# Kernel optimization log

Measured on AMD Instinct MI355X. Metric: run time of the kernel, lower is better.

Reference implementation:

```python
import jax, jax.numpy as jnp
import numpy as np

B, T, C = 2, 2048, 1024
NH = 16
DFF = 4096
EPS = 1e-5


def setup_inputs() -> dict:
    key = jax.random.key(0)
    ks = jax.random.split(key, 12)
    s = 0.02
    return {
        "x": jax.random.normal(ks[0], (B, T, C), dtype=jnp.float32),
        "Wq": jax.random.normal(ks[1], (C, C), dtype=jnp.float32) * s,
        "bq": jax.random.normal(ks[2], (C,), dtype=jnp.float32) * s,
        "Wk": jax.random.normal(ks[3], (C, C), dtype=jnp.float32) * s,
        "bk": jax.random.normal(ks[4], (C,), dtype=jnp.float32) * s,
        "Wv": jax.random.normal(ks[5], (C, C), dtype=jnp.float32) * s,
        "bv": jax.random.normal(ks[6], (C,), dtype=jnp.float32) * s,
        "W1": jax.random.normal(ks[7], (C, DFF), dtype=jnp.float32) * s,
        "b1": jax.random.normal(ks[8], (DFF,), dtype=jnp.float32) * s,
        "W2": jax.random.normal(ks[9], (DFF, C), dtype=jnp.float32) * s,
        "b2": jax.random.normal(ks[10], (C,), dtype=jnp.float32) * s,
        "ln_w": jnp.ones((C,), dtype=jnp.float32),
    }


def _layernorm(x, w):
    # LayerNorm over last dim, weight only (bias=False), eps=1e-5
    mu = jnp.mean(x, axis=-1, keepdims=True)
    var = jnp.mean(jnp.square(x - mu), axis=-1, keepdims=True)
    return (x - mu) / jnp.sqrt(var + EPS) * w


def reference(x, Wq, bq, Wk, bk, Wv, bv, W1, b1, W2, b2, ln_w):
    Bx, Tx, Cx = x.shape
    hd = Cx // NH
    q = (x @ Wq + bq).reshape(Bx, Tx, NH, hd).transpose(0, 2, 1, 3)  # [B,H,T,hd]
    k = (x @ Wk + bk).reshape(Bx, Tx, NH, hd).transpose(0, 2, 1, 3)
    v = (x @ Wv + bv).reshape(Bx, Tx, NH, hd).transpose(0, 2, 1, 3)
    # NOTE: original scales by sqrt(d_k) = sqrt(FULL model dim C), not head dim
    scores = jnp.einsum("bhqd,bhkd->bhqk", q, k) / jnp.sqrt(jnp.float32(Cx))
    causal = jnp.tril(jnp.ones((Tx, Tx), dtype=bool))
    scores = jnp.where(causal[None, None, :, :], scores, -jnp.inf)
    attn = jax.nn.softmax(scores, axis=-1)
    head_out = jnp.einsum("bhqk,bhkd->bhqd", attn, v)
    a = head_out.transpose(0, 2, 1, 3).reshape(Bx, Tx, Cx)
    # residuals: out = x + ln(x) with SHARED ln weight
    h = a + _layernorm(a, ln_w)
    f = jax.nn.relu(h @ W1 + b1) @ W2 + b2
    out = f + _layernorm(f, ln_w)
    return out
```

## Files before the change

kernel.cpp:

```cpp
#include <hip/hip_runtime.h>
#include <math.h>


typedef __attribute__((ext_vector_type(8))) short short8;
typedef __attribute__((ext_vector_type(4))) float f32x4;

__device__ __forceinline__ unsigned short f2bf(float f) {
    unsigned u = __builtin_bit_cast(unsigned, f);
    unsigned r = u + 0x7fffu + ((u >> 16) & 1u);
    return (unsigned short)(r >> 16);
}

__global__ __launch_bounds__(256) void convert_bf16_kernel(
    const float* __restrict__ in, unsigned short* __restrict__ out)
{
    const int i = (blockIdx.x * 256 + threadIdx.x) * 4;
    float4 v = *(const float4*)(in + i);
    ushort4 o;
    o.x = f2bf(v.x); o.y = f2bf(v.y); o.z = f2bf(v.z); o.w = f2bf(v.w);
    *(ushort4*)(out + i) = o;
}

__global__ __launch_bounds__(256) void transpose_convert_kernel(
    const float* __restrict__ in, unsigned short* __restrict__ out, int K, int N)
{
    __shared__ float tile[32][33];
    const int tx = threadIdx.x & 31;
    const int ty = threadIdx.x >> 5;
    const int n0 = blockIdx.x * 32;
    const int k0 = blockIdx.y * 32;
#pragma unroll
    for (int i = 0; i < 4; ++i)
        tile[ty + i * 8][tx] = in[(size_t)(k0 + ty + i * 8) * N + n0 + tx];
    __syncthreads();
#pragma unroll
    for (int i = 0; i < 4; ++i)
        out[(size_t)(n0 + ty + i * 8) * K + k0 + tx] = f2bf(tile[tx][ty + i * 8]);
}

__global__ __launch_bounds__(256) void concat2_kernel(
    const float* __restrict__ a, const float* __restrict__ b, float* __restrict__ o)
{
    const int i = blockIdx.x * 256 + threadIdx.x;
    o[i] = i < 1024 ? a[i] : b[i - 1024];
}

template <int TM, int TN>
__global__ __launch_bounds__(256) void gemm_bf16_mfma(
    const unsigned short* __restrict__ A, const unsigned short* __restrict__ Bt,
    const float* __restrict__ bias, float* __restrict__ Cf,
    unsigned short* __restrict__ Cb, int M, int N, int K, int mode)
{
    constexpr int NI = TM / 32;
    constexpr int NJ = TN / 32;
    constexpr int NA = TM / 64;
    constexpr int NB = TN / 64;

    __shared__ unsigned short As[TM * 32];
    __shared__ unsigned short Bs[TN * 32];

    const int tid  = threadIdx.x;
    const int lane = tid & 63;
    const int w    = tid >> 6;
    const int wm   = (w & 1) * (TM / 2);
    const int wn   = (w >> 1) * (TN / 2);
    const int fm   = lane & 15;
    const int quad = lane >> 4;

    const int row0 = blockIdx.y * TM;
    const int col0 = blockIdx.x * TN;

    const int srow = lane >> 2;
    const int scol = (lane & 3) * 8;

    const unsigned short* aptr[NA];
    unsigned short* alds[NA];
#pragma unroll
    for (int i = 0; i < NA; ++i) {
        const int r = (w * NA + i) * 16;
        aptr[i] = A + (size_t)(row0 + r + srow) * K + scol;
        alds[i] = &As[r * 32];
    }
    const unsigned short* bptr[NB];
    unsigned short* blds[NB];
#pragma unroll
    for (int i = 0; i < NB; ++i) {
        const int r = (w * NB + i) * 16;
        bptr[i] = Bt + (size_t)(col0 + r + srow) * K + scol;
        blds[i] = &Bs[r * 32];
    }

    f32x4 acc[NI][NJ] = {};

    for (int k0 = 0; k0 < K; k0 += 32) {
        __syncthreads();
#pragma unroll
        for (int i = 0; i < NA; ++i)
            __builtin_amdgcn_global_load_lds(
                (const __attribute__((address_space(1))) void*)(aptr[i] + k0),
                (__attribute__((address_space(3))) void*)alds[i], 16, 0, 0);
#pragma unroll
        for (int i = 0; i < NB; ++i)
            __builtin_amdgcn_global_load_lds(
                (const __attribute__((address_space(1))) void*)(bptr[i] + k0),
                (__attribute__((address_space(3))) void*)blds[i], 16, 0, 0);
        __syncthreads();

        short8 af[NI], bf[NJ];
#pragma unroll
        for (int i = 0; i < NI; ++i)
            af[i] = *(const short8*)&As[(wm + i * 16 + fm) * 32 + quad * 8];
#pragma unroll
        for (int j = 0; j < NJ; ++j)
            bf[j] = *(const short8*)&Bs[(wn + j * 16 + fm) * 32 + quad * 8];
#pragma unroll
        for (int i = 0; i < NI; ++i)
#pragma unroll
            for (int j = 0; j < NJ; ++j)
                acc[i][j] = __builtin_amdgcn_mfma_f32_16x16x32_bf16(
                    af[i], bf[j], acc[i][j], 0, 0, 0);
    }

#pragma unroll
    for (int j = 0; j < NJ; ++j) {
        const int col = col0 + wn + j * 16 + fm;
        const float bcol = (mode == 3) ? 0.f : bias[col];
#pragma unroll
        for (int i = 0; i < NI; ++i) {
            const int rbase = row0 + wm + i * 16 + quad * 4;
#pragma unroll
            for (int r = 0; r < 4; ++r) {
                const int row = rbase + r;
                float val = acc[i][j][r] + ((mode == 3) ? bias[row] : bcol);
                if (mode == 1) val = fmaxf(val, 0.f);
                if (mode == 0) Cf[(size_t)row * N + col] = val;
                else           Cb[(size_t)row * N + col] = f2bf(val);
            }
        }
    }
}

__global__ __launch_bounds__(256) void fattn_mfma(
    const unsigned short* __restrict__ qk,
    const unsigned short* __restrict__ vt,
    float* __restrict__ a)
{
    const int T = 2048, LDQK = 2048, LDVT = 4096, OUTC = 1024;
    const float cs = 0.04508422f;

    __shared__ unsigned short Qs[2][64][32];
    __shared__ unsigned short Ks[2][64][32];
    __shared__ unsigned short Vs[2][64][32];
    __shared__ unsigned short Ps[4][16][72];

    const int tid  = threadIdx.x;
    const int lane = tid & 63;
    const int w    = tid >> 6;
    const int fm   = lane & 15;
    const int quad = lane >> 4;
    const int srow = lane >> 2;
    const int scol = (lane & 3) * 8;

    const int n  = blockIdx.x;
    const int lo = n & 255, hi = n >> 8;
    const int h  = ((lo >> 5) & 7) | ((hi & 1) << 3);
    const int b  = hi >> 1;
    const int qv = lo & 31;
    const int u  = ((qv & 1) << 4) | ((qv & 2) << 2) | (qv & 4) |
                   ((qv & 8) >> 2) | ((qv & 16) >> 4);
    const int qb = (hi & 1) ? (31 - u) : u;
    const int q0 = qb * 64;

    const size_t rowbase = (size_t)b * T;

#pragma unroll
    for (int i = 0; i < 2; ++i) {
        const int c  = w * 2 + i;
        const int kh = c & 1, rg = c >> 1;
        const unsigned short* src = qk + (rowbase + q0 + rg * 16 + srow) * LDQK
                                       + h * 64 + kh * 32 + scol;
        __builtin_amdgcn_global_load_lds(
            (const __attribute__((address_space(1))) void*)src,
            (__attribute__((address_space(3))) void*)&Qs[kh][rg * 16][0], 16, 0, 0);
    }
    __syncthreads();
    short8 qf0 = *(const short8*)&Qs[0][w * 16 + fm][quad * 8];
    short8 qf1 = *(const short8*)&Qs[1][w * 16 + fm][quad * 8];

    short8 ones;
#pragma unroll
    for (int i = 0; i < 8; ++i) ones[i] = (short)0x3F80;

    f32x4 o[4] = {};
    f32x4 lacc = {};

    const int qglob = q0 + w * 16 + fm;

    for (int jt = 0; jt <= qb; ++jt) {
        const int j0 = jt * 64;
        __syncthreads();
#pragma unroll
        for (int i = 0; i < 2; ++i) {
            const int c  = w * 2 + i;
            const int kh = c & 1, rg = c >> 1;
            const unsigned short* ksrc = qk + (rowbase + j0 + rg * 16 + srow) * LDQK
                                            + 1024 + h * 64 + kh * 32 + scol;
            __builtin_amdgcn_global_load_lds(
                (const __attribute__((address_space(1))) void*)ksrc,
                (__attribute__((address_space(3))) void*)&Ks[kh][rg * 16][0], 16, 0, 0);
            const unsigned short* vsrc = vt + (size_t)(h * 64 + rg * 16 + srow) * LDVT
                                            + rowbase + j0 + kh * 32 + scol;
            __builtin_amdgcn_global_load_lds(
                (const __attribute__((address_space(1))) void*)vsrc,
                (__attribute__((address_space(3))) void*)&Vs[kh][rg * 16][0], 16, 0, 0);
        }
        __syncthreads();

        f32x4 s[4];
#pragma unroll
        for (int j = 0; j < 4; ++j) {
            short8 k0 = *(const short8*)&Ks[0][j * 16 + fm][quad * 8];
            short8 k1 = *(const short8*)&Ks[1][j * 16 + fm][quad * 8];
            f32x4 acc = {};
            acc = __builtin_amdgcn_mfma_f32_16x16x32_bf16(k0, qf0, acc, 0, 0, 0);
            acc = __builtin_amdgcn_mfma_f32_16x16x32_bf16(k1, qf1, acc, 0, 0, 0);
            s[j] = acc;
        }

        if (jt == qb) {
#pragma unroll
            for (int j = 0; j < 4; ++j) {
                const int kbase = j0 + j * 16 + quad * 4;
#pragma unroll
                for (int r = 0; r < 4; ++r) {
                    const float e = exp2f(s[j][r] * cs);
                    s[j][r] = (kbase + r > qglob) ? 0.f : e;
                }
            }
        } else {
#pragma unroll
            for (int j = 0; j < 4; ++j)
#pragma unroll
                for (int r = 0; r < 4; ++r)
                    s[j][r] = exp2f(s[j][r] * cs);
        }

#pragma unroll
        for (int j = 0; j < 4; ++j) {
            const unsigned d0 = (unsigned)f2bf(s[j][0]) | ((unsigned)f2bf(s[j][1]) << 16);
            const unsigned d1 = (unsigned)f2bf(s[j][2]) | ((unsigned)f2bf(s[j][3]) << 16);
            *(uint2*)&Ps[w][fm][j * 16 + quad * 4] = make_uint2(d0, d1);
        }
        short8 pf0 = *(const short8*)&Ps[w][fm][quad * 8];
        short8 pf1 = *(const short8*)&Ps[w][fm][32 + quad * 8];

#pragma unroll
        for (int jd = 0; jd < 4; ++jd) {
            short8 v0 = *(const short8*)&Vs[0][jd * 16 + fm][quad * 8];
            short8 v1 = *(const short8*)&Vs[1][jd * 16 + fm][quad * 8];
            o[jd] = __builtin_amdgcn_mfma_f32_16x16x32_bf16(pf0, v0, o[jd], 0, 0, 0);
            o[jd] = __builtin_amdgcn_mfma_f32_16x16x32_bf16(pf1, v1, o[jd], 0, 0, 0);
        }
        lacc = __builtin_amdgcn_mfma_f32_16x16x32_bf16(pf0, ones, lacc, 0, 0, 0);
        lacc = __builtin_amdgcn_mfma_f32_16x16x32_bf16(pf1, ones, lacc, 0, 0, 0);
    }

    const size_t orow = rowbase + q0 + w * 16 + quad * 4;
#pragma unroll
    for (int r = 0; r < 4; ++r) {
        const float inv = 1.0f / lacc[r];
#pragma unroll
        for (int jd = 0; jd < 4; ++jd)
            a[(orow + r) * OUTC + h * 64 + jd * 16 + fm] = o[jd][r] * inv;
    }
}

__global__ __launch_bounds__(256) void add_ln_kernel(
    const float* __restrict__ in, const float* __restrict__ w,
    float* __restrict__ outf, unsigned short* __restrict__ outb, int bf16_out)
{
    const int C = 1024;
    const int row = blockIdx.x;
    const int tid = threadIdx.x;

    __shared__ float red[256];

    const float* x = in + (size_t)row * C;
    float4 xv = *(const float4*)(x + tid * 4);

    red[tid] = xv.x + xv.y + xv.z + xv.w;
    __syncthreads();
    for (int off = 128; off > 0; off >>= 1) {
        if (tid < off) red[tid] += red[tid + off];
        __syncthreads();
    }
    const float mu = red[0] * (1.0f / 1024.0f);
    __syncthreads();

    float dx = xv.x - mu, dy = xv.y - mu, dz = xv.z - mu, dw = xv.w - mu;
    red[tid] = dx * dx + dy * dy + dz * dz + dw * dw;
    __syncthreads();
    for (int off = 128; off > 0; off >>= 1) {
        if (tid < off) red[tid] += red[tid + off];
        __syncthreads();
    }
    const float rstd = rsqrtf(red[0] * (1.0f / 1024.0f) + 1e-5f);

    float4 wv = *(const float4*)(w + tid * 4);
    float ox = xv.x + dx * rstd * wv.x;
    float oy = xv.y + dy * rstd * wv.y;
    float oz = xv.z + dz * rstd * wv.z;
    float ow = xv.w + dw * rstd * wv.w;
    if (bf16_out) {
        ushort4 o4;
        o4.x = f2bf(ox); o4.y = f2bf(oy); o4.z = f2bf(oz); o4.w = f2bf(ow);
        *(ushort4*)(outb + (size_t)row * C + tid * 4) = o4;
    } else {
        *(float4*)(outf + (size_t)row * C + tid * 4) = make_float4(ox, oy, oz, ow);
    }
}

extern "C" void kernel_launch(void* const* d_in, const int* in_sizes, int n_in,
                              void* d_out, int out_size, void* d_ws, size_t ws_size,
                              hipStream_t stream)
{
    const float* x    = (const float*)d_in[0];
    const float* Wq   = (const float*)d_in[1];
    const float* bq   = (const float*)d_in[2];
    const float* Wk   = (const float*)d_in[3];
    const float* bk   = (const float*)d_in[4];
    const float* Wv   = (const float*)d_in[5];
    const float* bv   = (const float*)d_in[6];
    const float* W1   = (const float*)d_in[7];
    const float* b1   = (const float*)d_in[8];
    const float* W2   = (const float*)d_in[9];
    const float* b2   = (const float*)d_in[10];
    const float* ln_w = (const float*)d_in[11];
    float* out = (float*)d_out;
    char* ws = (char*)d_ws;

    const int B = 2, T = 2048, C = 1024, DFF = 4096;
    const int M = B * T;
    const size_t MB = 1048576;

    unsigned short* qk_bf = (unsigned short*)(ws);
    unsigned short* vt_bf = (unsigned short*)(ws + 16 * MB);
    float*          a     = (float*)(ws + 24 * MB);
    unsigned short* x_bf  = (unsigned short*)(ws + 40 * MB);
    unsigned short* Wqk_t = (unsigned short*)(ws + 48 * MB);
    unsigned short* Wvt   = (unsigned short*)(ws + 52 * MB);
    unsigned short* W1t   = (unsigned short*)(ws + 54 * MB);
    unsigned short* W2t   = (unsigned short*)(ws + 62 * MB);
    float*          bqk   = (float*)(ws + 70 * MB);
    unsigned short* u_bf  = (unsigned short*)(ws + 71 * MB);
    unsigned short* h_bf  = x_bf;
    float*          f     = (float*)(ws);

    dim3 blk(256);

    convert_bf16_kernel<<<dim3(M * C / 1024), blk, 0, stream>>>(x, x_bf);
    transpose_convert_kernel<<<dim3(32, 32), blk, 0, stream>>>(Wq, Wqk_t, C, C);
    transpose_convert_kernel<<<dim3(32, 32), blk, 0, stream>>>(Wk, Wqk_t + 1024 * 1024, C, C);
    transpose_convert_kernel<<<dim3(32, 32), blk, 0, stream>>>(Wv, Wvt, C, C);
    transpose_convert_kernel<<<dim3(128, 32), blk, 0, stream>>>(W1, W1t, C, DFF);
    transpose_convert_kernel<<<dim3(32, 128), blk, 0, stream>>>(W2, W2t, DFF, C);
    concat2_kernel<<<dim3(8), blk, 0, stream>>>(bq, bk, bqk);

    gemm_bf16_mfma<64, 128><<<dim3(2 * C / 128, M / 64), blk, 0, stream>>>(
        x_bf, Wqk_t, bqk, nullptr, qk_bf, M, 2 * C, C, 2);

    gemm_bf16_mfma<64, 64><<<dim3(M / 64, C / 64), blk, 0, stream>>>(
        Wvt, x_bf, bv, nullptr, vt_bf, C, M, C, 3);

    fattn_mfma<<<dim3(1024), blk, 0, stream>>>(qk_bf, vt_bf, a);

    add_ln_kernel<<<dim3(M), blk, 0, stream>>>(a, ln_w, nullptr, h_bf, 1);

    gemm_bf16_mfma<128, 128><<<dim3(DFF / 128, M / 128), blk, 0, stream>>>(
        h_bf, W1t, b1, nullptr, u_bf, M, DFF, C, 1);

    gemm_bf16_mfma<64, 64><<<dim3(C / 64, M / 64), blk, 0, stream>>>(
        u_bf, W2t, b2, f, nullptr, M, C, DFF, 0);

    add_ln_kernel<<<dim3(M), blk, 0, stream>>>(f, ln_w, out, nullptr, 0);
}
```

Measured before the change: 374.0 us.

## Split-K the W2 GEMM in two and fuse partial-sum reduction into LayerNorm

The second FFN GEMM (K=4096) is launched with a z-dimension of 2. Each half computes a partial product over K/2 and writes fp32 partials to separate buffers. A new add_ln2 kernel sums the two partials plus the b2 bias before the residual LayerNorm. This aims to double the block count and shorten the per-block K loop for better CU occupancy, at the cost of extra fp32 partial traffic.

```diff
diff --git a/kernel.cpp b/kernel.cpp
--- a/kernel.cpp
+++ b/kernel.cpp
@@ -49,7 +49,8 @@
 __global__ __launch_bounds__(256) void gemm_bf16_mfma(
     const unsigned short* __restrict__ A, const unsigned short* __restrict__ Bt,
     const float* __restrict__ bias, float* __restrict__ Cf,
-    unsigned short* __restrict__ Cb, int M, int N, int K, int mode)
+    unsigned short* __restrict__ Cb, int M, int N, int K, int lda, int ldb,
+    int mode)
 {
     constexpr int NI = TM / 32;
     constexpr int NJ = TN / 32;
@@ -69,6 +70,7 @@
 
     const int row0 = blockIdx.y * TM;
     const int col0 = blockIdx.x * TN;
+    const int koff = blockIdx.z * K;
 
     const int srow = lane >> 2;
     const int scol = (lane & 3) * 8;
@@ -78,7 +80,7 @@
 #pragma unroll
     for (int i = 0; i < NA; ++i) {
         const int r = (w * NA + i) * 16;
-        aptr[i] = A + (size_t)(row0 + r + srow) * K + scol;
+        aptr[i] = A + (size_t)(row0 + r + srow) * lda + koff + scol;
         alds[i] = &As[r * 32];
     }
     const unsigned short* bptr[NB];
@@ -86,7 +88,7 @@
 #pragma unroll
     for (int i = 0; i < NB; ++i) {
         const int r = (w * NB + i) * 16;
-        bptr[i] = Bt + (size_t)(col0 + r + srow) * K + scol;
+        bptr[i] = Bt + (size_t)(col0 + r + srow) * ldb + koff + scol;
         blds[i] = &Bs[r * 32];
     }
 
@@ -121,10 +123,11 @@
                     af[i], bf[j], acc[i][j], 0, 0, 0);
     }
 
+    const size_t zoff = (mode == 4) ? (size_t)blockIdx.z * M * N : 0;
 #pragma unroll
     for (int j = 0; j < NJ; ++j) {
         const int col = col0 + wn + j * 16 + fm;
-        const float bcol = (mode == 3) ? 0.f : bias[col];
+        const float bcol = (mode == 3 || mode == 4) ? 0.f : bias[col];
 #pragma unroll
         for (int i = 0; i < NI; ++i) {
             const int rbase = row0 + wm + i * 16 + quad * 4;
@@ -133,8 +136,8 @@
                 const int row = rbase + r;
                 float val = acc[i][j][r] + ((mode == 3) ? bias[row] : bcol);
                 if (mode == 1) val = fmaxf(val, 0.f);
-                if (mode == 0) Cf[(size_t)row * N + col] = val;
-                else           Cb[(size_t)row * N + col] = f2bf(val);
+                if (mode == 0 || mode == 4) Cf[zoff + (size_t)row * N + col] = val;
+                else                        Cb[(size_t)row * N + col] = f2bf(val);
             }
         }
     }
@@ -318,6 +321,50 @@
     } else {
         *(float4*)(outf + (size_t)row * C + tid * 4) = make_float4(ox, oy, oz, ow);
     }
+}
+
+__global__ __launch_bounds__(256) void add_ln2_kernel(
+    const float* __restrict__ p0, const float* __restrict__ p1,
+    const float* __restrict__ b2, const float* __restrict__ w,
+    float* __restrict__ out)
+{
+    const int C = 1024;
+    const int row = blockIdx.x;
+    const int tid = threadIdx.x;
+
+    __shared__ float red[256];
+
+    float4 v0 = *(const float4*)(p0 + (size_t)row * C + tid * 4);
+    float4 v1 = *(const float4*)(p1 + (size_t)row * C + tid * 4);
+    float4 bb = *(const float4*)(b2 + tid * 4);
+    float4 xv = make_float4(v0.x + v1.x + bb.x, v0.y + v1.y + bb.y,
+                            v0.z + v1.z + bb.z, v0.w + v1.w + bb.w);
+
+    red[tid] = xv.x + xv.y + xv.z + xv.w;
+    __syncthreads();
+    for (int off = 128; off > 0; off >>= 1) {
+        if (tid < off) red[tid] += red[tid + off];
+        __syncthreads();
+    }
+    const float mu = red[0] * (1.0f / 1024.0f);
+    __syncthreads();
+
+    float dx = xv.x - mu, dy = xv.y - mu, dz = xv.z - mu, dw = xv.w - mu;
+    red[tid] = dx * dx + dy * dy + dz * dz + dw * dw;
+    __syncthreads();
+    for (int off = 128; off > 0; off >>= 1) {
+        if (tid < off) red[tid] += red[tid + off];
+        __syncthreads();
+    }
+    const float rstd = rsqrtf(red[0] * (1.0f / 1024.0f) + 1e-5f);
+
+    float4 wv = *(const float4*)(w + tid * 4);
+    float4 o;
+    o.x = xv.x + dx * rstd * wv.x;
+    o.y = xv.y + dy * rstd * wv.y;
+    o.z = xv.z + dz * rstd * wv.z;
+    o.w = xv.w + dw * rstd * wv.w;
+    *(float4*)(out + (size_t)row * C + tid * 4) = o;
 }
 
 extern "C" void kernel_launch(void* const* d_in, const int* in_sizes, int n_in,
@@ -354,7 +401,7 @@
     float*          bqk   = (float*)(ws + 70 * MB);
     unsigned short* u_bf  = (unsigned short*)(ws + 71 * MB);
     unsigned short* h_bf  = x_bf;
-    float*          f     = (float*)(ws);
+    float*          pK    = (float*)(ws);
 
     dim3 blk(256);
 
@@ -367,20 +414,21 @@
     concat2_kernel<<<dim3(8), blk, 0, stream>>>(bq, bk, bqk);
 
     gemm_bf16_mfma<64, 128><<<dim3(2 * C / 128, M / 64), blk, 0, stream>>>(
-        x_bf, Wqk_t, bqk, nullptr, qk_bf, M, 2 * C, C, 2);
+        x_bf, Wqk_t, bqk, nullptr, qk_bf, M, 2 * C, C, C, C, 2);
 
     gemm_bf16_mfma<64, 64><<<dim3(M / 64, C / 64), blk, 0, stream>>>(
-        Wvt, x_bf, bv, nullptr, vt_bf, C, M, C, 3);
+        Wvt, x_bf, bv, nullptr, vt_bf, C, M, C, C, C, 3);
 
     fattn_mfma<<<dim3(1024), blk, 0, stream>>>(qk_bf, vt_bf, a);
 
     add_ln_kernel<<<dim3(M), blk, 0, stream>>>(a, ln_w, nullptr, h_bf, 1);
 
     gemm_bf16_mfma<128, 128><<<dim3(DFF / 128, M / 128), blk, 0, stream>>>(
-        h_bf, W1t, b1, nullptr, u_bf, M, DFF, C, 1);
-
-    gemm_bf16_mfma<64, 64><<<dim3(C / 64, M / 64), blk, 0, stream>>>(
-        u_bf, W2t, b2, f, nullptr, M, C, DFF, 0);
-
-    add_ln_kernel<<<dim3(M), blk, 0, stream>>>(f, ln_w, out, nullptr, 0);
-}
+        h_bf, W1t, b1, nullptr, u_bf, M, DFF, C, C, C, 1);
+
+    gemm_bf16_mfma<64, 64><<<dim3(C / 64, M / 64, 2), blk, 0, stream>>>(
+        u_bf, W2t, nullptr, pK, nullptr, M, C, DFF / 2, DFF, DFF, 4);
+
+    add_ln2_kernel<<<dim3(M), blk, 0, stream>>>(
+        pK, pK + (size_t)M * C, b2, ln_w, out);
+}
```

Result: slower. 391.2 us (+4.6%).
